# Performance work log

Measured on AMD Instinct MI355X. Metric: run time of the kernel, lower is better.

## Reference

```python
import jax, jax.numpy as jnp
import numpy as np

N, L, C = 4, 1024, 512   # batch, frames, channels (in_channels == mdl_channels)
H = 16                   # heads
D = C // H               # head dim
S = 16                   # number of segments for bi
EPS_PN = 1e-5            # MaskPowerNorm / GroupScaling eps


def setup_inputs() -> dict:
    key = jax.random.key(0)
    ks = jax.random.split(key, 8)
    x = jax.random.normal(ks[0], (N, L, C), jnp.float32)
    bi = jnp.sort(jax.random.randint(ks[1], (L,), 0, S)).astype(jnp.int64)
    w_qkv = jax.random.normal(ks[2], (3 * C, C), jnp.float32) * 0.02
    w_beta = jax.random.normal(ks[3], (1, 3 * C), jnp.float32) * 0.02
    w1 = jax.random.normal(ks[4], (C, C), jnp.float32) * 0.02
    b1 = jnp.zeros((C,), jnp.float32)
    w2 = jax.random.normal(ks[5], (C, C), jnp.float32) * 0.02
    b2 = jnp.zeros((C,), jnp.float32)
    pn1_w = jnp.ones((C,), jnp.float32)
    pn1_b = jnp.zeros((C,), jnp.float32)
    pn1_phi = jnp.ones((C,), jnp.float32)
    pn2_w = jnp.ones((C,), jnp.float32)
    pn2_b = jnp.zeros((C,), jnp.float32)
    pn2_phi = jnp.ones((C,), jnp.float32)
    return dict(x=x, bi=bi, w_qkv=w_qkv, w_beta=w_beta, w1=w1, b1=b1, w2=w2,
                b2=b2, pn1_w=pn1_w, pn1_b=pn1_b, pn1_phi=pn1_phi,
                pn2_w=pn2_w, pn2_b=pn2_b, pn2_phi=pn2_phi)


def power_norm(x, weight, bias, running_phi):
    # MaskPowerNorm (eval): GroupScaling1D over H channel groups, then
    # x / sqrt(running_phi + eps) * weight + bias
    n, l, c = x.shape
    cg = c // H
    g = x.reshape(n, l, H, cg)
    m2 = jnp.mean(g * g, axis=-1, keepdims=True)
    gs = (g / jnp.sqrt(m2 + EPS_PN)).reshape(n, l, c)
    return gs / jnp.sqrt(running_phi + EPS_PN) * weight + bias


def reference(x, bi, w_qkv, w_beta, w1, b1, w2, b2,
              pn1_w, pn1_b, pn1_phi, pn2_w, pn2_b, pn2_phi):
    n, l, c = x.shape
    d = c // H
    # QKV projection (bias=False)
    qkv = x @ w_qkv.T                                  # (n, l, 3c)
    q, k, v = jnp.split(qkv, 3, axis=-1)
    q = q.reshape(n, l, H, d)
    k = k.reshape(n, l, H, d)
    v = v.reshape(n, l, H, d)
    # elu feature map on temperature-scaled q, k
    temp = d ** (-0.25)
    phi = lambda t: jax.nn.elu(t * temp) + 1.0
    q = phi(q).transpose(0, 2, 1, 3)                   # (n, h, l, d)
    k = phi(k).transpose(0, 2, 1, 3)                   # (n, h, l, d)
    vt = v.transpose(0, 2, 1, 3)                       # (n, h, l, d)
    # per-position outer products k v^T : (n, h, l, d, d)
    kv = k[..., :, None] * vt[..., None, :]
    # scatter_sum over frames into S segments, then gather back per frame
    kv_seg = jnp.zeros((n, H, S, d, d), kv.dtype).at[:, :, bi].add(kv)
    kv_g = kv_seg[:, :, bi]                            # (n, h, l, d, d)
    k_seg = jnp.zeros((n, H, S, d), k.dtype).at[:, :, bi].add(k)
    k_g = k_seg[:, :, bi]                              # (n, h, l, d)
    z = 1.0 / jnp.sum(q * k_g, axis=-1)                # (n, h, l)
    v_out = jnp.einsum('nhld,nhldm->nhlm', q, kv_g) * z[..., None]
    t = v_out.transpose(0, 2, 1, 3).reshape(n, l, c)   # (n, l, c)
    # AddNorm with beta gate (dropout is identity in eval)
    beta = jax.nn.sigmoid(jnp.concatenate([t, x, t - x], axis=-1) @ w_beta.T)
    x1 = power_norm(beta * x + (1.0 - beta) * t, pn1_w, pn1_b, pn1_phi)
    # FFN (exact GELU) + AddNorm (no beta)
    ff = jax.nn.gelu(x1 @ w1.T + b1, approximate=False) @ w2.T + b2
    return power_norm(ff + x1, pn2_w, pn2_b, pn2_phi)
```

## Files before the change

kernel.cpp:

```cpp
#include <hip/hip_runtime.h>
#include <math.h>

#define NB 4
#define LB 1024
#define CB 512
#define HH 16
#define DD 32
#define SS 16
#define NL (NB*LB)
#define C3 (3*CB)

typedef __attribute__((ext_vector_type(8))) short short8;
typedef __attribute__((ext_vector_type(4))) float f32x4;

#define GL16(gp, lp) __builtin_amdgcn_global_load_lds( \
    (const __attribute__((address_space(1))) void*)(gp), \
    (__attribute__((address_space(3))) void*)(lp), 16, 0, 0)

__device__ __forceinline__ unsigned short f2bf_rn(float f) {
  unsigned u = __builtin_bit_cast(unsigned, f);
  unsigned r = u + 0x7FFFu + ((u >> 16) & 1u);
  return (unsigned short)(r >> 16);
}
__device__ __forceinline__ float bf2f(unsigned short h) {
  unsigned u = ((unsigned)h) << 16;
  return __builtin_bit_cast(float, u);
}

__device__ __forceinline__ int lower_bound_i32(const int* a, int n, int v) {
  int lo = 0, hi = n;
  while (lo < hi) { int mid = (lo + hi) >> 1; if (a[mid] < v) lo = mid + 1; else hi = mid; }
  return lo;
}

#define X4T   524288
#define WQ4T  720896
#define W14T  786432
#define TOT4  851968
__global__ __launch_bounds__(256) void split_conv(
    const float* __restrict__ x, const float* __restrict__ wqkv,
    const float* __restrict__ w1, const float* __restrict__ w2,
    ushort* __restrict__ xh, ushort* __restrict__ xl,
    ushort* __restrict__ wqh, ushort* __restrict__ wql,
    ushort* __restrict__ w1h, ushort* __restrict__ w1l,
    ushort* __restrict__ w2h, ushort* __restrict__ w2l)
{
  for (int idx = blockIdx.x * 256 + threadIdx.x; idx < TOT4; idx += gridDim.x * 256) {
    const float* src; ushort *dh, *dl; int off;
    if (idx < X4T)        { src = x;    dh = xh;  dl = xl;  off = idx; }
    else if (idx < WQ4T)  { src = wqkv; dh = wqh; dl = wql; off = idx - X4T; }
    else if (idx < W14T)  { src = w1;   dh = w1h; dl = w1l; off = idx - WQ4T; }
    else                  { src = w2;   dh = w2h; dl = w2l; off = idx - W14T; }
    const float4 v = ((const float4*)src)[off];
    ushort4 h, l;
    h.x = f2bf_rn(v.x); l.x = f2bf_rn(v.x - bf2f(h.x));
    h.y = f2bf_rn(v.y); l.y = f2bf_rn(v.y - bf2f(h.y));
    h.z = f2bf_rn(v.z); l.z = f2bf_rn(v.z - bf2f(h.z));
    h.w = f2bf_rn(v.w); l.w = f2bf_rn(v.w - bf2f(h.w));
    ((ushort4*)dh)[off] = h;
    ((ushort4*)dl)[off] = l;
  }
}

template<int MODE, int BM, int BN>
__global__ __launch_bounds__(256) void gemm_mfma3(
    const ushort* __restrict__ Ah, const ushort* __restrict__ Al,
    const ushort* __restrict__ Bh, const ushort* __restrict__ Bl,
    int M, int Nn, int K,
    const float* __restrict__ bias,
    float* __restrict__ Cf, ushort* __restrict__ Ch, ushort* __restrict__ Cl,
    const ushort* __restrict__ resh, const ushort* __restrict__ resl)
{
  constexpr int MI = BM / 32;
  constexpr int NJ = BN / 32;
  constexpr int ASLOT = BM * 4;
  constexpr int BSLOT = BN * 4;
  __shared__ short8 AhL[2*ASLOT], AlL[2*ASLOT];
  __shared__ short8 BhL[2*BSLOT], BlL[2*BSLOT];
  const int tid = threadIdx.x;
  const int w = tid >> 6, l = tid & 63;
  const int wm = w >> 1, wn = w & 1;
  const int l15 = l & 15, l4 = l >> 4;
  const int bm = blockIdx.x * BM, bn = blockIdx.y * BN;

  f32x4 acc[MI][NJ];
  #pragma unroll
  for (int i = 0; i < MI; ++i)
    #pragma unroll
    for (int j = 0; j < NJ; ++j)
      acc[i][j] = {0.f, 0.f, 0.f, 0.f};

  const int NT = K / 32;

  auto stage = [&](int buf, int k0) {
    #pragma unroll
    for (int i = 0; i < ASLOT/256; ++i) {
      const int pb = buf*ASLOT + i*256 + w*64;
      const int p  = i*256 + w*64 + l;
      const long go = (long)(bm + (p & (BM-1))) * K + k0 + (p / BM) * 8;
      GL16(Ah + go, (char*)AhL + pb*16);
      GL16(Al + go, (char*)AlL + pb*16);
    }
    #pragma unroll
    for (int i = 0; i < BSLOT/256; ++i) {
      const int pb = buf*BSLOT + i*256 + w*64;
      const int p  = i*256 + w*64 + l;
      const long go = (long)(bn + (p & (BN-1))) * K + k0 + (p / BN) * 8;
      GL16(Bh + go, (char*)BhL + pb*16);
      GL16(Bl + go, (char*)BlL + pb*16);
    }
  };

  stage(0, 0);
  __syncthreads();
  int cur = 0;
  for (int t = 0; t < NT; ++t) {
    if (t + 1 < NT) stage(cur ^ 1, (t + 1) * 32);
    short8 bhf[NJ], blf[NJ];
    #pragma unroll
    for (int j = 0; j < NJ; ++j) {
      const int idx = cur*BSLOT + l4*BN + wn*(BN/2) + j*16 + l15;
      bhf[j] = BhL[idx]; blf[j] = BlL[idx];
    }
    #pragma unroll
    for (int i = 0; i < MI; ++i) {
      const int idx = cur*ASLOT + l4*BM + wm*(BM/2) + i*16 + l15;
      const short8 ah = AhL[idx], al = AlL[idx];
      #pragma unroll
      for (int j = 0; j < NJ; ++j) {
        acc[i][j] = __builtin_amdgcn_mfma_f32_16x16x32_bf16(ah, bhf[j], acc[i][j], 0, 0, 0);
        acc[i][j] = __builtin_amdgcn_mfma_f32_16x16x32_bf16(ah, blf[j], acc[i][j], 0, 0, 0);
        acc[i][j] = __builtin_amdgcn_mfma_f32_16x16x32_bf16(al, bhf[j], acc[i][j], 0, 0, 0);
      }
    }
    __syncthreads();
    cur ^= 1;
  }

  const float temp = 0.42044820762685725f;
  #pragma unroll
  for (int i = 0; i < MI; ++i) {
    #pragma unroll
    for (int j = 0; j < NJ; ++j) {
      const int n  = bn + wn * (BN/2) + j * 16 + l15;
      const int mb = bm + wm * (BM/2) + i * 16 + l4 * 4;
      #pragma unroll
      for (int r = 0; r < 4; ++r) {
        const int m = mb + r;
        float v = acc[i][j][r];
        if (MODE == 0) {
          if (n < 2 * CB) { const float z = v * temp; v = (z > 0.f) ? (z + 1.f) : expf(z); }
          Cf[(long)m * Nn + n] = v;
        } else if (MODE == 1) {
          v += bias[n];
          v = v * 0.5f * (1.f + erff(v * 0.70710678118654752f));
          const ushort hb = f2bf_rn(v);
          Ch[(long)m * Nn + n] = hb;
          Cl[(long)m * Nn + n] = f2bf_rn(v - bf2f(hb));
        } else {
          const long o = (long)m * Nn + n;
          v += bias[n] + bf2f(resh[o]) + bf2f(resl[o]);
          Cf[o] = v;
        }
      }
    }
  }
}

__global__ __launch_bounds__(256) void seg_attn(
    const float* __restrict__ qkv, const int* __restrict__ bi,
    float* __restrict__ tbuf)
{
  const int b = blockIdx.x;
  const int s = b & (SS-1);
  const int h = (b >> 4) & (HH-1);
  const int n = b >> 8;
  __shared__ float ks[32][DD];
  __shared__ float vs[32][DD];
  __shared__ float KVs[DD][DD];
  __shared__ float Ks[DD];
  __shared__ int sb[2];
  const int tid = threadIdx.x;
  if (tid == 0) {
    sb[0] = lower_bound_i32(bi, LB, s);
    sb[1] = lower_bound_i32(bi, LB, s + 1);
  }
  __syncthreads();
  const int lo = sb[0], hi = sb[1];
  const int srow = tid >> 3, sq = tid & 7;
  const int d = tid >> 3, m0 = (tid & 7) * 4;
  float4 acc = make_float4(0.f, 0.f, 0.f, 0.f);
  float ksum = 0.f;

  for (int l0 = lo; l0 < hi; l0 += 32) {
    const int lr = l0 + srow;
    if (lr < hi) {
      const float* row = qkv + (long)(n*LB + lr) * C3 + h*DD;
      *(float4*)&ks[srow][sq*4] = *(const float4*)(row + CB   + sq*4);
      *(float4*)&vs[srow][sq*4] = *(const float4*)(row + 2*CB + sq*4);
    } else {
      *(float4*)&ks[srow][sq*4] = make_float4(0.f,0.f,0.f,0.f);
      *(float4*)&vs[srow][sq*4] = make_float4(0.f,0.f,0.f,0.f);
    }
    __syncthreads();
    #pragma unroll
    for (int r = 0; r < 32; ++r) {
      const float kd = ks[r][d];
      ksum += kd;
      const float4 vv = *(const float4*)&vs[r][m0];
      acc.x = fmaf(kd, vv.x, acc.x);
      acc.y = fmaf(kd, vv.y, acc.y);
      acc.z = fmaf(kd, vv.z, acc.z);
      acc.w = fmaf(kd, vv.w, acc.w);
    }
    __syncthreads();
  }
  *(float4*)&KVs[d][m0] = acc;
  if ((tid & 7) == 0) Ks[d] = ksum;
  __syncthreads();

  const int prow = tid >> 5, m = tid & 31;
  for (int l0 = lo; l0 < hi; l0 += 32) {
    const int lr = l0 + srow;
    if (lr < hi)
      *(float4*)&ks[srow][sq*4] = *(const float4*)(qkv + (long)(n*LB + lr) * C3 + h*DD + sq*4);
    __syncthreads();
    #pragma unroll
    for (int step = 0; step < 4; ++step) {
      const int r  = step * 8 + prow;
      const int l2 = l0 + r;
      if (l2 < hi) {
        float vo = 0.f, den = 0.f;
        #pragma unroll
        for (int d2 = 0; d2 < DD; ++d2) {
          const float qd = ks[r][d2];
          vo  = fmaf(qd, KVs[d2][m], vo);
          den = fmaf(qd, Ks[d2], den);
        }
        tbuf[(long)(n*LB + l2) * CB + h*DD + m] = vo / den;
      }
    }
    __syncthreads();
  }
}

__global__ __launch_bounds__(256) void beta_pn1(
    const float* __restrict__ x, const float* __restrict__ tbuf,
    const float* __restrict__ w_beta,
    const float* __restrict__ pw, const float* __restrict__ pb, const float* __restrict__ pphi,
    ushort* __restrict__ x1h, ushort* __restrict__ x1l)
{
  const int row = blockIdx.x;
  const int tid = threadIdx.x;
  const int c0 = tid * 2;
  const long base = (long)row * CB;
  const float2 xv = *(const float2*)&x[base + c0];
  const float2 tv = *(const float2*)&tbuf[base + c0];
  float p = tv.x * w_beta[c0]   + xv.x * w_beta[CB + c0]   + (tv.x - xv.x) * w_beta[2*CB + c0]
          + tv.y * w_beta[c0+1] + xv.y * w_beta[CB + c0+1] + (tv.y - xv.y) * w_beta[2*CB + c0+1];
  #pragma unroll
  for (int off = 32; off >= 1; off >>= 1) p += __shfl_xor(p, off, 64);
  __shared__ float red[4];
  if ((tid & 63) == 0) red[tid >> 6] = p;
  __syncthreads();
  const float zsum = red[0] + red[1] + red[2] + red[3];
  const float beta = 1.f / (1.f + expf(-zsum));
  const float y0 = beta * xv.x + (1.f - beta) * tv.x;
  const float y1 = beta * xv.y + (1.f - beta) * tv.y;
  float ss = y0*y0 + y1*y1;
  #pragma unroll
  for (int off = 1; off < 16; off <<= 1) ss += __shfl_xor(ss, off, 64);
  const float inv = rsqrtf(ss * (1.f/32.f) + 1e-5f);
  const float o0 = y0 * inv * rsqrtf(pphi[c0]   + 1e-5f) * pw[c0]   + pb[c0];
  const float o1 = y1 * inv * rsqrtf(pphi[c0+1] + 1e-5f) * pw[c0+1] + pb[c0+1];
  const ushort h0 = f2bf_rn(o0), h1 = f2bf_rn(o1);
  const ushort g0 = f2bf_rn(o0 - bf2f(h0)), g1 = f2bf_rn(o1 - bf2f(h1));
  *(ushort2*)&x1h[base + c0] = make_ushort2(h0, h1);
  *(ushort2*)&x1l[base + c0] = make_ushort2(g0, g1);
}

__global__ __launch_bounds__(256) void pn2_kernel(
    const float* __restrict__ ffx,
    const float* __restrict__ pw, const float* __restrict__ pb, const float* __restrict__ pphi,
    float* __restrict__ out)
{
  const int row = blockIdx.x;
  const int tid = threadIdx.x;
  const int c0 = tid * 2;
  const long base = (long)row * CB;
  const float2 yv = *(const float2*)&ffx[base + c0];
  float ss = yv.x*yv.x + yv.y*yv.y;
  #pragma unroll
  for (int off = 1; off < 16; off <<= 1) ss += __shfl_xor(ss, off, 64);
  const float inv = rsqrtf(ss * (1.f/32.f) + 1e-5f);
  const float o0 = yv.x * inv * rsqrtf(pphi[c0]   + 1e-5f) * pw[c0]   + pb[c0];
  const float o1 = yv.y * inv * rsqrtf(pphi[c0+1] + 1e-5f) * pw[c0+1] + pb[c0+1];
  *(float2*)&out[base + c0] = make_float2(o0, o1);
}

extern "C" void kernel_launch(void* const* d_in, const int* in_sizes, int n_in,
                              void* d_out, int out_size, void* d_ws, size_t ws_size,
                              hipStream_t stream)
{
  const float* x       = (const float*)d_in[0];
  const int*   bi      = (const int*)d_in[1];
  const float* w_qkv   = (const float*)d_in[2];
  const float* w_beta  = (const float*)d_in[3];
  const float* w1      = (const float*)d_in[4];
  const float* b1      = (const float*)d_in[5];
  const float* w2      = (const float*)d_in[6];
  const float* b2      = (const float*)d_in[7];
  const float* pn1_w   = (const float*)d_in[8];
  const float* pn1_b   = (const float*)d_in[9];
  const float* pn1_phi = (const float*)d_in[10];
  const float* pn2_w   = (const float*)d_in[11];
  const float* pn2_b   = (const float*)d_in[12];
  const float* pn2_phi = (const float*)d_in[13];
  float* out = (float*)d_out;
  char*  wsb = (char*)d_ws;

  ushort* wqh  = (ushort*)(wsb);
  ushort* wql  = (ushort*)(wsb +  1572864);
  ushort* w1h  = (ushort*)(wsb +  3145728);
  ushort* w1l  = (ushort*)(wsb +  3670016);
  ushort* w2h  = (ushort*)(wsb +  4194304);
  ushort* w2l  = (ushort*)(wsb +  4718592);
  ushort* xh   = (ushort*)(wsb +  5242880);
  ushort* xl   = (ushort*)(wsb +  9437184);
  float*  tbuf = (float*) (wsb +  5242880);
  float*  qkvb = (float*) (wsb + 13631488);
  ushort* x1h  = (ushort*)(wsb + 13631488);
  ushort* x1l  = (ushort*)(wsb + 17825792);
  ushort* h1h  = (ushort*)(wsb + 22020096);
  ushort* h1l  = (ushort*)(wsb + 26214400);
  float*  ffx  = (float*) (wsb + 30408704);

  split_conv<<<2048, 256, 0, stream>>>(x, w_qkv, w1, w2,
                                       xh, xl, wqh, wql, w1h, w1l, w2h, w2l);
  gemm_mfma3<0,128,128><<<dim3(NL/128, C3/128), 256, 0, stream>>>(
      xh, xl, wqh, wql, NL, C3, CB, nullptr, qkvb, nullptr, nullptr, nullptr, nullptr);
  seg_attn<<<NB*HH*SS, 256, 0, stream>>>(qkvb, bi, tbuf);
  beta_pn1<<<NL, 256, 0, stream>>>(x, tbuf, w_beta, pn1_w, pn1_b, pn1_phi, x1h, x1l);
  gemm_mfma3<1,64,64><<<dim3(NL/64, CB/64), 256, 0, stream>>>(
      x1h, x1l, w1h, w1l, NL, CB, CB, b1, nullptr, h1h, h1l, nullptr, nullptr);
  gemm_mfma3<2,64,64><<<dim3(NL/64, CB/64), 256, 0, stream>>>(
      h1h, h1l, w2h, w2l, NL, CB, CB, b2, ffx, nullptr, nullptr, x1h, x1l);
  pn2_kernel<<<NL, 256, 0, stream>>>(ffx, pn2_w, pn2_b, pn2_phi, out);
}
```

Before: 204.2 us.

## Drop LDS double buffering in split-bf16 GEMM and shrink QKV tile to 128x64

Replaces the double-buffered LDS prefetch pipeline in the 3-pass bf16 MFMA GEMM with a single buffer: each K-step loads, syncs, then computes. This halves LDS use per block, which may allow more resident blocks and hide latency through occupancy instead of explicit prefetch. The QKV projection tile also shrinks from 128x128 to 128x64, doubling its grid. The cost is no overlap of global loads with MFMA work inside a block, plus an extra barrier per K-step.

```diff
diff --git a/kernel.cpp b/kernel.cpp
--- a/kernel.cpp
+++ b/kernel.cpp
@@ -63,7 +63,7 @@
 }
 
 template<int MODE, int BM, int BN>
-__global__ __launch_bounds__(256) void gemm_mfma3(
+__global__ __launch_bounds__(256) void gemm_mfma4(
     const ushort* __restrict__ Ah, const ushort* __restrict__ Al,
     const ushort* __restrict__ Bh, const ushort* __restrict__ Bl,
     int M, int Nn, int K,
@@ -75,8 +75,8 @@
   constexpr int NJ = BN / 32;
   constexpr int ASLOT = BM * 4;
   constexpr int BSLOT = BN * 4;
-  __shared__ short8 AhL[2*ASLOT], AlL[2*ASLOT];
-  __shared__ short8 BhL[2*BSLOT], BlL[2*BSLOT];
+  __shared__ short8 AhL[ASLOT], AlL[ASLOT];
+  __shared__ short8 BhL[BSLOT], BlL[BSLOT];
   const int tid = threadIdx.x;
   const int w = tid >> 6, l = tid & 63;
   const int wm = w >> 1, wn = w & 1;
@@ -90,41 +90,35 @@
     for (int j = 0; j < NJ; ++j)
       acc[i][j] = {0.f, 0.f, 0.f, 0.f};
 
-  const int NT = K / 32;
-
-  auto stage = [&](int buf, int k0) {
+  for (int k0 = 0; k0 < K; k0 += 32) {
+    if (k0) __syncthreads();
     #pragma unroll
     for (int i = 0; i < ASLOT/256; ++i) {
-      const int pb = buf*ASLOT + i*256 + w*64;
-      const int p  = i*256 + w*64 + l;
+      const int pb = i*256 + w*64;
+      const int p  = pb + l;
       const long go = (long)(bm + (p & (BM-1))) * K + k0 + (p / BM) * 8;
       GL16(Ah + go, (char*)AhL + pb*16);
       GL16(Al + go, (char*)AlL + pb*16);
     }
     #pragma unroll
     for (int i = 0; i < BSLOT/256; ++i) {
-      const int pb = buf*BSLOT + i*256 + w*64;
-      const int p  = i*256 + w*64 + l;
+      const int pb = i*256 + w*64;
+      const int p  = pb + l;
       const long go = (long)(bn + (p & (BN-1))) * K + k0 + (p / BN) * 8;
       GL16(Bh + go, (char*)BhL + pb*16);
       GL16(Bl + go, (char*)BlL + pb*16);
     }
-  };
-
-  stage(0, 0);
-  __syncthreads();
-  int cur = 0;
-  for (int t = 0; t < NT; ++t) {
-    if (t + 1 < NT) stage(cur ^ 1, (t + 1) * 32);
+    __syncthreads();
+
     short8 bhf[NJ], blf[NJ];
     #pragma unroll
     for (int j = 0; j < NJ; ++j) {
-      const int idx = cur*BSLOT + l4*BN + wn*(BN/2) + j*16 + l15;
+      const int idx = l4*BN + wn*(BN/2) + j*16 + l15;
       bhf[j] = BhL[idx]; blf[j] = BlL[idx];
     }
     #pragma unroll
     for (int i = 0; i < MI; ++i) {
-      const int idx = cur*ASLOT + l4*BM + wm*(BM/2) + i*16 + l15;
+      const int idx = l4*BM + wm*(BM/2) + i*16 + l15;
       const short8 ah = AhL[idx], al = AlL[idx];
       #pragma unroll
       for (int j = 0; j < NJ; ++j) {
@@ -133,8 +127,6 @@
         acc[i][j] = __builtin_amdgcn_mfma_f32_16x16x32_bf16(al, bhf[j], acc[i][j], 0, 0, 0);
       }
     }
-    __syncthreads();
-    cur ^= 1;
   }
 
   const float temp = 0.42044820762685725f;
@@ -337,13 +329,13 @@
 
   split_conv<<<2048, 256, 0, stream>>>(x, w_qkv, w1, w2,
                                        xh, xl, wqh, wql, w1h, w1l, w2h, w2l);
-  gemm_mfma3<0,128,128><<<dim3(NL/128, C3/128), 256, 0, stream>>>(
+  gemm_mfma4<0,128,64><<<dim3(NL/128, C3/64), 256, 0, stream>>>(
       xh, xl, wqh, wql, NL, C3, CB, nullptr, qkvb, nullptr, nullptr, nullptr, nullptr);
   seg_attn<<<NB*HH*SS, 256, 0, stream>>>(qkvb, bi, tbuf);
   beta_pn1<<<NL, 256, 0, stream>>>(x, tbuf, w_beta, pn1_w, pn1_b, pn1_phi, x1h, x1l);
-  gemm_mfma3<1,64,64><<<dim3(NL/64, CB/64), 256, 0, stream>>>(
+  gemm_mfma4<1,64,64><<<dim3(NL/64, CB/64), 256, 0, stream>>>(
       x1h, x1l, w1h, w1l, NL, CB, CB, b1, nullptr, h1h, h1l, nullptr, nullptr);
-  gemm_mfma3<2,64,64><<<dim3(NL/64, CB/64), 256, 0, stream>>>(
+  gemm_mfma4<2,64,64><<<dim3(NL/64, CB/64), 256, 0, stream>>>(
       h1h, h1l, w2h, w2l, NL, CB, CB, b2, ffx, nullptr, nullptr, x1h, x1l);
   pn2_kernel<<<NL, 256, 0, stream>>>(ffx, pn2_w, pn2_b, pn2_phi, out);
 }
```

Measured after the change: 211.3 us. +3.4%, slower.
